# Performance work log

Measured on AMD Instinct MI355X. Metric: run time of the kernel, lower is better.

The kernel has to match this reference:

```python
import jax, jax.numpy as jnp
import numpy as np
from jax import lax

D = 300   # dim (hidden_size)
T = 1024  # grown history length
B = 128   # batched independent steps


def _conv(x, w, b):
    # NCHW conv, 3x3, stride 1, SAME padding (matches nn.Conv2d(.,.,3,1,1))
    return lax.conv_general_dilated(x, w, (1, 1), 'SAME',
                                    dimension_numbers=('NCHW', 'OIHW', 'NCHW')) + b[None, :, None, None]


def _bn(x, g, b, eps=1e-5):
    # eval-mode BatchNorm2d with running_mean=0, running_var=1
    return x * (g / jnp.sqrt(1.0 + eps))[None, :, None, None] + b[None, :, None, None]


def setup_inputs():
    key = jax.random.key(0)
    ks = iter(jax.random.split(key, 64))
    def rn(shape, scale=1.0):
        return jax.random.normal(next(ks), shape, dtype=jnp.float32) * scale
    inp = {
        'x': rn((B, D)),
        'hidden_states': rn((B, T, D)),
        'past_ht': rn((B, T, D)),
        'past_c': rn((B, T, D)),
        'W': rn((4 * D, 2 * D), 0.05),
        'b': rn((4 * D,)).at[:D].set(1.0),   # self.b[:dim] = 1
        'W_h': rn((10, D), 0.1),
        'W_x': rn((10, D), 0.1),
        'W_ht': rn((10, D), 0.1),
        'v': rn((10,)),
        'rb_w': rn((1600, 4 * D), 0.02),  # reshape_bef: Linear(1200, 1600)
        'rb_b': rn((1600,), 0.02),
        'rp_w': rn((4 * D, 1600), 0.02),  # reshape_pos: Linear(1600, 1200)
        'rp_b': rn((4 * D,), 0.02),
    }
    chans = [(1, 32), (32, 64), (64, 64), (64, 64), (64, 32), (32, 1)]
    for i, (ci, co) in enumerate(chans, 1):
        inp[f'c{i}_w'] = rn((co, ci, 3, 3), 0.1)
        inp[f'c{i}_b'] = rn((co,), 0.02)
        inp[f'c{i}_g'] = jnp.ones((co,), jnp.float32)
        inp[f'c{i}_beta'] = jnp.zeros((co,), jnp.float32)
    inp['pc_w'] = rn((1, 2, 3, 3), 0.1)
    inp['pc_b'] = rn((1,), 0.02)
    inp['pc_g'] = jnp.ones((1,), jnp.float32)
    inp['pc_beta'] = jnp.zeros((1,), jnp.float32)
    return inp


def reference(x, hidden_states, past_ht, past_c, W, b, W_h, W_x, W_ht, v,
              rb_w, rb_b, rp_w, rp_b,
              c1_w, c1_b, c1_g, c1_beta, c2_w, c2_b, c2_g, c2_beta,
              c3_w, c3_b, c3_g, c3_beta, c4_w, c4_b, c4_g, c4_beta,
              c5_w, c5_b, c5_g, c5_beta, c6_w, c6_b, c6_g, c6_beta,
              pc_w, pc_b, pc_g, pc_beta):
    # --- intra-attention over the grown history (vectorized over k) ---
    # a_k = v @ tanh(W_h h_k + W_x x + W_ht pht_k)
    e = jnp.tanh(jnp.einsum('btd,kd->btk', hidden_states, W_h)
                 + jnp.einsum('bd,kd->bk', x, W_x)[:, None, :]
                 + jnp.einsum('btd,kd->btk', past_ht, W_ht))
    s = jax.nn.softmax(jnp.einsum('btk,k->bt', e, v), axis=-1)
    ht = jnp.einsum('bt,btd->bd', s, hidden_states)
    ct = jnp.einsum('bt,btd->bd', s, past_c)
    # --- gate pre-activations ---
    whx = jnp.concatenate([ht, x], axis=-1) @ W.T + b          # [B, 1200]
    whx = whx @ rb_w.T + rb_b                                  # [B, 1600]
    pre = whx.reshape(-1, 1, 40, 40)
    # --- inter conv block (dropout is identity in eval) ---
    y = pre
    for (w, bi, g, be) in ((c1_w, c1_b, c1_g, c1_beta), (c2_w, c2_b, c2_g, c2_beta),
                           (c3_w, c3_b, c3_g, c3_beta), (c4_w, c4_b, c4_g, c4_beta),
                           (c5_w, c5_b, c5_g, c5_beta), (c6_w, c6_b, c6_g, c6_beta)):
        y = _bn(jax.nn.relu(_conv(y, w, bi)), g, be)
    y = _bn(_conv(jnp.concatenate([pre, y], axis=1), pc_w, pc_b), pc_g, pc_beta)
    whx = y.reshape(-1, 1600) @ rp_w.T + rp_b                  # [B, 1200]
    # --- LSTM gating ---
    f_t = jax.nn.sigmoid(whx[:, :D])
    o_t = jax.nn.sigmoid(whx[:, D:2 * D])
    i_t = jax.nn.sigmoid(whx[:, 2 * D:3 * D])
    ch_t = jnp.tanh(whx[:, 3 * D:4 * D])
    c = f_t * ct + i_t * ch_t
    h = o_t * jnp.tanh(c)
    return h
```

## Files before the change

kernel.cpp:

```cpp
#include <hip/hip_runtime.h>
#include <hip/hip_bf16.h>
#include <cstdint>
#include <cstddef>

typedef unsigned short u16;
typedef unsigned int u32;

#define DEV __device__ __forceinline__

DEV float bf2f(u16 u){ union{unsigned int i; float f;} c; c.i = ((unsigned)u)<<16; return c.f; }
DEV u16 f2bf(float f){ union{float f;unsigned int i;} c; c.f=f; unsigned int r = c.i + 0x7FFFu + ((c.i>>16)&1u); return (u16)(r>>16); }
DEV unsigned int pk2(float a, float b){
  __hip_bfloat162 t = __float22bfloat162_rn(float2{a,b});
  union { __hip_bfloat162 h; unsigned int u; } cv; cv.h = t; return cv.u;
}

typedef __attribute__((ext_vector_type(8))) short bf16x8;
typedef __attribute__((ext_vector_type(4))) float f32x4;
typedef __attribute__((ext_vector_type(8))) unsigned short us8v;

static constexpr size_t OFF_XW    = 0;
static constexpr size_t OFF_WHX2  = 8192;
static constexpr size_t OFF_WHX3  = OFF_WHX2 + (size_t)128*1600*4;
static constexpr size_t OFF_W21   = OFF_WHX3 + (size_t)128*1200*4;
static constexpr size_t OFF_WB2   = OFF_W21  + (size_t)288*4;
static constexpr size_t OFF_WB3   = OFF_WB2  + (size_t)18432*2;
static constexpr size_t OFF_WB4   = OFF_WB3  + (size_t)36864*2;
static constexpr size_t OFF_WB5   = OFF_WB4  + (size_t)36864*2;
static constexpr size_t OFF_W26   = OFF_WB5  + (size_t)18432*2;
static constexpr size_t OFF_PAR   = OFF_W26  + (size_t)288*4;
static constexpr size_t OFF_WPACK = OFF_PAR  + (size_t)6*768;
static constexpr size_t OFF_WB1G  = OFF_WPACK+ (size_t)20480*2;
static constexpr size_t OFF_RBWB  = OFF_WB1G + (size_t)1216*608*2;
static constexpr size_t OFF_RPWB  = OFF_RBWB + (size_t)1600*1216*2;
static constexpr size_t OFF_CAT   = OFF_RPWB + (size_t)1216*1600*2;
static constexpr size_t OFF_WHX1B = OFF_CAT  + (size_t)128*608*2;
static constexpr size_t OFF_O16B  = OFF_WHX1B+ (size_t)128*1216*2;
static constexpr size_t OFF_CT    = OFF_O16B + (size_t)128*1600*2;
static constexpr size_t OFF_A32   = OFF_CT   + (size_t)128*300*4;
static constexpr size_t OFF_B64   = OFF_A32  + (size_t)128*1764*32*2;
static constexpr size_t OFF_C64   = OFF_B64  + (size_t)128*1764*64*2;
static constexpr size_t OFF_P0    = OFF_C64  + (size_t)128*1764*64*2;
static constexpr size_t OFF_Y6    = OFF_P0   + (size_t)128*1764*2;
static constexpr size_t OFF_PART  = OFF_C64;

DEV void ring0(u16* buf, int j){
  int b = j/164, i = j%164;
  int y, x;
  if      (i < 42){ y = 0;        x = i; }
  else if (i < 84){ y = 41;       x = i-42; }
  else if (i < 124){ y = i-84+1;  x = 0; }
  else             { y = i-124+1; x = 41; }
  buf[(size_t)b*1764 + y*42 + x] = 0;
}
__global__ __launch_bounds__(256) void zero_mega(u16* __restrict__ p0, u16* __restrict__ y6,
                                                 u16* __restrict__ catb){
  int id = blockIdx.x*256 + threadIdx.x;
  if (id < 20992) ring0(p0, id);
  else if (id < 41984) ring0(y6, id-20992);
  else if (id < 42112){
    int b = id - 41984;
    us8v z = {0,0,0,0,0,0,0,0};
    *(us8v*)(catb + (size_t)b*608 + 600) = z;
  }
}

struct RArgs {
  const float* cw[6]; const float* cb[6]; const float* cg[6]; const float* cbe[6];
  const float* Wh; const float* Wht; const float* Wg; const float* rbw; const float* rpw;
  float* w21; float* w26; float* par;
  u16 *wb2, *wb3, *wb4, *wb5, *wpack, *Wb1, *rbwb, *rpwb;
};
DEV void cvW(const float* w, u16* dst, size_t j, int CI){
  int ci = j % CI; size_t rem = j / CI; int dydx = rem % 9; int co = rem / 9;
  dst[j] = f2bf(w[((size_t)co*CI + ci)*9 + dydx]);
}
__global__ __launch_bounds__(256) void mega_repack(RArgs a){
  const float isc = 1.0f/sqrtf(1.00001f);
  for (size_t id = (size_t)blockIdx.x*256 + threadIdx.x; id < 4762947ull;
       id += (size_t)gridDim.x*256){
    if (id < 288){
      int co = id % 32; size_t rem = id / 32; int k = rem % 9;
      a.w21[id] = a.cw[0][co*9 + k];
    } else if (id < 18720){ cvW(a.cw[1], a.wb2, id-288, 32); }
    else if (id < 55584){ cvW(a.cw[2], a.wb3, id-18720, 64); }
    else if (id < 92448){ cvW(a.cw[3], a.wb4, id-55584, 64); }
    else if (id < 110880){ cvW(a.cw[4], a.wb5, id-92448, 64); }
    else if (id < 111168){
      size_t j = id - 110880;
      a.w26[j] = a.cw[5][j];
    } else if (id < 131648){
      size_t j = id - 111168;
      int jj = j&7, col=(int)((j>>3)&15), kg=(int)((j>>7)&3); size_t rest=j>>9;
      int ks = (int)(rest%10), tz = (int)(rest/10);
      int k = ks*32 + kg*8 + jj;
      const float* src = tz ? a.Wht : a.Wh;
      a.wpack[j] = f2bf((col<10 && k<300)? src[col*300+k] : 0.f);
    } else if (id < 870976){
      size_t j = id - 131648; int k = (int)(j % 608); int n = (int)(j / 608);
      a.Wb1[j] = f2bf((n<1200 && k<600)? a.Wg[(size_t)n*600+k] : 0.f);
    } else if (id < 2816576){
      size_t j = id - 870976; int k = (int)(j % 1216); int n = (int)(j / 1216);
      a.rbwb[j] = f2bf((k<1200)? a.rbw[(size_t)n*1200+k] : 0.f);
    } else if (id < 4762176){
      size_t j = id - 2816576; int k = (int)(j % 1600); int n = (int)(j / 1600);
      a.rpwb[j] = f2bf((n<1200)? a.rpw[(size_t)n*1600+k] : 0.f);
    } else {
      size_t j = id - 4762176;
      int ci, CO; size_t base;
      if (j < 96){ ci=0; CO=32; base=0; }
      else if (j < 288){ ci=1; CO=64; base=96; }
      else if (j < 480){ ci=2; CO=64; base=288; }
      else if (j < 672){ ci=3; CO=64; base=480; }
      else if (j < 768){ ci=4; CO=32; base=672; }
      else { ci=5; CO=1; base=768; }
      size_t jj = j - base; int t = (int)(jj / CO); int c = (int)(jj % CO);
      float* p = a.par + (size_t)ci*192;
      p[t*CO + c] = (t==0)? a.cb[ci][c] : (t==1)? a.cg[ci][c]*isc : a.cbe[ci][c];
    }
  }
}

__global__ __launch_bounds__(64) void xw_k(const float* __restrict__ x, const float* __restrict__ Wx,
                                           float* __restrict__ xw){
  int id = blockIdx.x;
  int b = id/10, k = id%10;
  int lane = threadIdx.x;
  float a = 0.f;
  for (int d = lane; d < 300; d += 64)
    a = fmaf(x[b*300+d], Wx[k*300+d], a);
  #pragma unroll
  for (int off=1; off<64; off<<=1) a += __shfl_xor(a, off);
  if (lane==0) xw[b*16+k] = a;
}

__global__ __launch_bounds__(256,3) void attn_fused(const float* __restrict__ hs, const float* __restrict__ pht,
    const float* __restrict__ pc, const u16* __restrict__ wpack, const float* __restrict__ v,
    const float* __restrict__ xw, float* __restrict__ part){
  __shared__ u16 HL[32][328];
  __shared__ u16 PL[32][328];
  __shared__ float PS[2][32][18];
  __shared__ float PP[32];
  __shared__ float ML[2];
  int tid = threadIdx.x;
  int chunk = blockIdx.x, b = blockIdx.y;
  int rr0 = (b<<10) + chunk*32;
  const float* hsrc = hs  + (size_t)rr0*300;
  const float* psrc = pht + (size_t)rr0*300;
  const float* csrc = pc  + (size_t)rr0*300;
  float4 creg[10];
  #pragma unroll
  for (int rnd=0; rnd<10; rnd++){
    int idx = rnd*256 + tid;
    if (idx < 2400) creg[rnd] = *(const float4*)(csrc + idx*4);
  }
  #pragma unroll
  for (int rnd=0; rnd<10; rnd++){
    int idx = rnd*256 + tid;
    if (idx < 2400){
      float4 qh = *(const float4*)(hsrc + idx*4);
      float4 qp = *(const float4*)(psrc + idx*4);
      int row = idx/75, colp = (idx - row*75)*4;
      uint2 pvh; pvh.x = pk2(qh.x,qh.y); pvh.y = pk2(qh.z,qh.w);
      uint2 pvp; pvp.x = pk2(qp.x,qp.y); pvp.y = pk2(qp.z,qp.w);
      *(uint2*)(&HL[row][colp]) = pvh;
      *(uint2*)(&PL[row][colp]) = pvp;
    }
  }
  #pragma unroll
  for (int j=0;j<2;j++){
    int idx = j*256 + tid;
    if (idx < 448){
      int row = idx/14, cc = 300 + (idx - row*14)*2;
      *(u32*)(&HL[row][cc]) = 0u;
      *(u32*)(&PL[row][cc]) = 0u;
    }
  }
  __syncthreads();
  {
    int w = tid>>6, l = tid&63;
    int c = l&15, g = l>>4;
    int tz = w>>1, rf = w&1;
    const u16 (*SL)[328] = tz ? PL : HL;
    const u16* wbase = wpack + (size_t)tz*5120;
    f32x4 acc = (f32x4){0.f,0.f,0.f,0.f};
    #pragma unroll
    for (int ks=0; ks<10; ks++){
      bf16x8 af  = *(const bf16x8*)(&SL[rf*16 + c][ks*32 + g*8]);
      bf16x8 bfr = *(const bf16x8*)(wbase + ((ks*4 + g)*16 + c)*8);
      acc = __builtin_amdgcn_mfma_f32_16x16x32_bf16(af, bfr, acc, 0, 0, 0);
    }
    #pragma unroll
    for (int r=0;r<4;r++) PS[tz][rf*16 + g*4 + r][c] = acc[r];
  }
  __syncthreads();
  #pragma unroll
  for (int rnd=0; rnd<10; rnd++){
    int idx = rnd*256 + tid;
    if (idx < 2400){
      int row = idx/75, colp = (idx - row*75)*4;
      uint2 pv; pv.x = pk2(creg[rnd].x, creg[rnd].y); pv.y = pk2(creg[rnd].z, creg[rnd].w);
      *(uint2*)(&PL[row][colp]) = pv;
    }
  }
  if (tid < 32){
    float s = 0.f;
    #pragma unroll
    for (int k=0;k<10;k++)
      s += v[k]*tanhf(PS[0][tid][k] + PS[1][tid][k] + xw[b*16+k]);
    float m = s;
    #pragma unroll
    for (int off=1; off<32; off<<=1) m = fmaxf(m, __shfl_xor(m, off));
    float p = expf(s - m);
    float l = p;
    #pragma unroll
    for (int off=1; off<32; off<<=1) l += __shfl_xor(l, off);
    PP[tid] = p;
    if (tid==0){ ML[0]=m; ML[1]=l; }
  }
  __syncthreads();
  float* pp = part + ((size_t)b*32 + chunk)*608;
  if (tid < 150){
    int d = tid*2;
    float h0=0,h1=0,c0=0,c1=0;
    #pragma unroll
    for (int t=0;t<32;t++){
      float p = PP[t];
      u32 hw = *(const u32*)(&HL[t][d]);
      u32 cw = *(const u32*)(&PL[t][d]);
      h0 = fmaf(p, bf2f((u16)hw),       h0);
      h1 = fmaf(p, bf2f((u16)(hw>>16)), h1);
      c0 = fmaf(p, bf2f((u16)cw),       c0);
      c1 = fmaf(p, bf2f((u16)(cw>>16)), c1);
    }
    *(float2*)(pp + 4 + d)   = float2{h0,h1};
    *(float2*)(pp + 308 + d) = float2{c0,c1};
  }
  if (tid==0){ pp[0]=ML[0]; pp[1]=ML[1]; }
}

__global__ __launch_bounds__(192) void attn_reduce(const float* __restrict__ part,
    const float* __restrict__ x, float* __restrict__ ct, u16* __restrict__ catb){
  int b = blockIdx.x;
  int tid = threadIdx.x;
  const float* pb = part + (size_t)b*32*608;
  float M = -3.0e38f;
  #pragma unroll
  for (int j=0;j<32;j++) M = fmaxf(M, pb[j*608]);
  float L = 0.f;
  #pragma unroll
  for (int j=0;j<32;j++) L += pb[j*608+1]*expf(pb[j*608]-M);
  if (tid < 150){
    int d = tid*2;
    float a0=0,a1=0,b0=0,b1=0;
    #pragma unroll
    for (int j=0;j<32;j++){
      float w = expf(pb[j*608]-M);
      float2 hh = *(const float2*)(pb + j*608 + 4 + d);
      float2 cc = *(const float2*)(pb + j*608 + 308 + d);
      a0 = fmaf(w,hh.x,a0); a1 = fmaf(w,hh.y,a1);
      b0 = fmaf(w,cc.x,b0); b1 = fmaf(w,cc.y,b1);
    }
    float inv = 1.f/L;
    *(float2*)(ct + (size_t)b*300 + d) = float2{b0*inv, b1*inv};
    *(u32*)(catb + (size_t)b*608 + d)       = pk2(a0*inv, a1*inv);
    *(u32*)(catb + (size_t)b*608 + 300 + d) = pk2(x[(size_t)b*300 + d], x[(size_t)b*300 + d + 1]);
  }
}

template<int KP, bool OUTBF>
__global__ __launch_bounds__(256) void gemm_mfma(int NW, int NB, int ldo,
    const u16* __restrict__ inB, const u16* __restrict__ Wb,
    const float* __restrict__ bias, void* __restrict__ outp){
  __shared__ float red[4][64][4];
  int w = threadIdx.x>>6, l = threadIdx.x&63;
  int c = l&15, g = l>>4;
  int n0 = blockIdx.x*16;
  int b0 = blockIdx.y*16;
  const u16* arow = Wb  + (size_t)(n0 + c)*KP + g*8;
  const u16* brow = inB + (size_t)(b0 + c)*KP + g*8;
  f32x4 acc = (f32x4){0.f,0.f,0.f,0.f};
  for (int ks = w; ks < KP/32; ks += 4){
    bf16x8 af = *(const bf16x8*)(arow + ks*32);
    bf16x8 bf = *(const bf16x8*)(brow + ks*32);
    acc = __builtin_amdgcn_mfma_f32_16x16x32_bf16(af, bf, acc, 0, 0, 0);
  }
  #pragma unroll
  for (int r=0;r<4;r++) red[w][l][r] = acc[r];
  __syncthreads();
  if (w==0){
    float s0 = red[0][l][0]+red[1][l][0]+red[2][l][0]+red[3][l][0];
    float s1 = red[0][l][1]+red[1][l][1]+red[2][l][1]+red[3][l][1];
    float s2 = red[0][l][2]+red[1][l][2]+red[2][l][2]+red[3][l][2];
    float s3 = red[0][l][3]+red[1][l][3]+red[2][l][3]+red[3][l][3];
    int b = b0 + c, nb = n0 + g*4;
    if (nb < NW){
      float4 bi;
      if (nb < NB) bi = *(const float4*)(bias + nb);
      else { bi.x=0; bi.y=0; bi.z=0; bi.w=0; }
      float o0=s0+bi.x, o1=s1+bi.y, o2=s2+bi.z, o3=s3+bi.w;
      if (OUTBF){
        ushort4 st; st.x=f2bf(o0); st.y=f2bf(o1); st.z=f2bf(o2); st.w=f2bf(o3);
        *(ushort4*)((u16*)outp + (size_t)b*ldo + nb) = st;
      } else {
        float4 st; st.x=o0; st.y=o1; st.z=o2; st.w=o3;
        *(float4*)((float*)outp + (size_t)b*ldo + nb) = st;
      }
    }
  }
}

DEV void bzero(u16* buf, int j, int CH, int C){
  int c8 = j % CH; int rem = j / CH;
  int i = rem % 164, b = rem / 164;
  int y, x;
  if      (i < 42){ y = 0;        x = i; }
  else if (i < 84){ y = 41;       x = i-42; }
  else if (i < 124){ y = i-84+1;  x = 0; }
  else             { y = i-124+1; x = 41; }
  us8v z = {0,0,0,0,0,0,0,0};
  *(us8v*)(buf + ((size_t)b*1764 + y*42 + x)*C + c8*8) = z;
}
__global__ __launch_bounds__(256) void scat_border(const float* __restrict__ whx2, u16* __restrict__ p0,
    u16* __restrict__ A32, u16* __restrict__ B64, u16* __restrict__ C64){
  int id = blockIdx.x*256 + threadIdx.x;
  if (id < 204800){
    int b = id/1600, p = id%1600;
    int y = p/40, x = p%40;
    p0[(size_t)b*1764 + (y+1)*42 + (x+1)] = f2bf(whx2[id]);
  } else if (id < 288768){ bzero(A32, id-204800, 4, 32); }
  else if (id < 456704){ bzero(B64, id-288768, 8, 64); }
  else { bzero(C64, id-456704, 8, 64); }
}

template<int CI, int CO>
__global__ __launch_bounds__(256) void conv_tile(const u16* __restrict__ in, u16* __restrict__ out,
    const u16* __restrict__ wB, const float* __restrict__ par){
  constexpr int PCI  = CI + 8;
  constexpr int MF   = CO/16;
  constexpr int FPW  = MF;
  constexpr int KC   = CI/32;
  constexpr int KROW = CI*9;
  constexpr int CH8  = CI/8;
  __shared__ u16 TIN[100*PCI];
  int tile = blockIdx.x;
  int b = blockIdx.y;
  int y0 = (tile/5)*8, x0 = (tile%5)*8;
  const u16* inb = in + (size_t)b*1764*CI;
  for (int g = threadIdx.x; g < 100*CH8; g += 256){
    int pix = g/CH8, ch = g - pix*CH8;
    int r = pix/10, cc = pix - r*10;
    us8v vdat = *(const us8v*)(inb + ((size_t)(y0+r)*42 + (x0+cc))*CI + ch*8);
    *(us8v*)(&TIN[pix*PCI + ch*8]) = vdat;
  }
  __syncthreads();
  int w = threadIdx.x>>6, l = threadIdx.x&63;
  int c = l&15, kg = l>>4;
  int mg, f0;
  if (MF==4){ mg = w; f0 = 0; } else { mg = w&1; f0 = (w>>1)*2; }
  int pxb[FPW];
  #pragma unroll
  for (int fi=0; fi<FPW; fi++){
    int px = (f0+fi)*16 + c;
    int ty = px>>3, tx = px&7;
    pxb[fi] = (ty*10 + tx)*PCI + kg*8;
  }
  const u16* wrow = wB + (size_t)(mg*16 + c)*KROW;
  f32x4 acc[FPW];
  #pragma unroll
  for (int fi=0; fi<FPW; fi++) acc[fi] = (f32x4){0.f,0.f,0.f,0.f};
  #pragma unroll
  for (int dy=0;dy<3;dy++)
  #pragma unroll
  for (int dx=0;dx<3;dx++){
    int dydx = dy*3+dx;
    #pragma unroll
    for (int kc=0; kc<KC; kc++){
      bf16x8 af = *(const bf16x8*)(wrow + dydx*CI + kc*32 + kg*8);
      #pragma unroll
      for (int fi=0; fi<FPW; fi++){
        bf16x8 bf = *(const bf16x8*)(&TIN[pxb[fi] + (dy*10+dx)*PCI + kc*32]);
        acc[fi] = __builtin_amdgcn_mfma_f32_16x16x32_bf16(af, bf, acc[fi], 0, 0, 0);
      }
    }
  }
  u16* ob = out + (size_t)b*1764*CO;
  int co0 = mg*16 + kg*4;
  const float4 bia = *(const float4*)(par + co0);
  const float4 sc  = *(const float4*)(par + CO + co0);
  const float4 be  = *(const float4*)(par + 2*CO + co0);
  #pragma unroll
  for (int fi=0; fi<FPW; fi++){
    int px = (f0+fi)*16 + c;
    int y = y0 + (px>>3), x = x0 + (px&7);
    ushort4 s;
    s.x = f2bf(fmaxf(acc[fi][0]+bia.x,0.f)*sc.x + be.x);
    s.y = f2bf(fmaxf(acc[fi][1]+bia.y,0.f)*sc.y + be.y);
    s.z = f2bf(fmaxf(acc[fi][2]+bia.z,0.f)*sc.z + be.z);
    s.w = f2bf(fmaxf(acc[fi][3]+bia.w,0.f)*sc.w + be.w);
    *(ushort4*)(ob + (size_t)((y+1)*42 + (x+1))*CO + co0) = s;
  }
}

template<int CI, int CO, bool TT>
__global__ __launch_bounds__(256) void conv_main(const u16* __restrict__ in, u16* __restrict__ out,
    const float* __restrict__ w2, const float* __restrict__ par){
  int b = blockIdx.x;
  int wave = threadIdx.x >> 6;
  int lane = threadIdx.x & 63;
  int tile, co;
  if (TT){ tile = blockIdx.y*8 + wave*2 + (lane>>5); co = lane & 31; }
  else   { tile = blockIdx.y*4 + wave;               co = lane; }
  int y0 = (tile >> 3)*5, x0 = (tile & 7)*5;
  const u16* inb = in + (size_t)b*1764*CI;
  float acc[25];
  #pragma unroll
  for (int p=0;p<25;p++) acc[p]=0.f;
  for (int ci=0; ci<CI; ci++){
    float win[49];
    #pragma unroll
    for (int r=0;r<7;r++)
      #pragma unroll
      for (int c=0;c<7;c++)
        win[r*7+c] = bf2f(inb[ ((y0+r)*42 + (x0+c))*CI + ci ]);
    float wk[9];
    #pragma unroll
    for (int k=0;k<9;k++) wk[k] = w2[(ci*9+k)*CO + co];
    #pragma unroll
    for (int py=0;py<5;py++)
      #pragma unroll
      for (int px=0;px<5;px++){
        float s = acc[py*5+px];
        #pragma unroll
        for (int dy=0;dy<3;dy++)
          #pragma unroll
          for (int dx=0;dx<3;dx++)
            s = fmaf(wk[dy*3+dx], win[(py+dy)*7 + (px+dx)], s);
        acc[py*5+px] = s;
      }
  }
  float bia = par[co], sc = par[CO+co], be = par[2*CO+co];
  u16* outb = out + (size_t)b*1764*CO;
  #pragma unroll
  for (int py=0;py<5;py++)
    #pragma unroll
    for (int px=0;px<5;px++){
      float vv = fmaxf(acc[py*5+px] + bia, 0.f)*sc + be;
      outb[ ((y0+py+1)*42 + (x0+px+1))*CO + co ] = f2bf(vv);
    }
}

__global__ __launch_bounds__(256) void conv_c6(const u16* __restrict__ in, u16* __restrict__ y6,
    const float* __restrict__ w6, const float* __restrict__ par6){
  int id = blockIdx.x*256 + threadIdx.x;
  int b = id/1600, p = id%1600;
  int y = p/40, x = p%40;
  const u16* inb = in + (size_t)b*1764*32;
  float acc = 0.f;
  #pragma unroll
  for (int dy=0;dy<3;dy++)
    #pragma unroll
    for (int dx=0;dx<3;dx++){
      const u16* q = inb + ((y+dy)*42 + (x+dx))*32;
      int k = dy*3+dx;
      #pragma unroll
      for (int g=0; g<4; g++){
        us8v vv8 = *(const us8v*)(q + g*8);
        #pragma unroll
        for (int j=0;j<8;j++)
          acc = fmaf(w6[(g*8+j)*9 + k], bf2f(vv8[j]), acc);
      }
    }
  float vv = fmaxf(acc + par6[0], 0.f)*par6[1] + par6[2];
  y6[(size_t)b*1764 + (y+1)*42 + (x+1)] = f2bf(vv);
}

__global__ __launch_bounds__(256) void conv_pc(const u16* __restrict__ p0, const u16* __restrict__ y6,
    const float* __restrict__ pcw, const float* __restrict__ pcb,
    const float* __restrict__ pcg, const float* __restrict__ pcbe,
    u16* __restrict__ o16b){
  int id = blockIdx.x*256 + threadIdx.x;
  int b = id/1600, p = id%1600;
  int y = p/40, x = p%40;
  float acc = 0.f;
  #pragma unroll
  for (int dy=0;dy<3;dy++)
    #pragma unroll
    for (int dx=0;dx<3;dx++){
      size_t o = (size_t)b*1764 + (y+dy)*42 + (x+dx);
      acc = fmaf(pcw[dy*3+dx],     bf2f(p0[o]), acc);
      acc = fmaf(pcw[9 + dy*3+dx], bf2f(y6[o]), acc);
    }
  float sc = pcg[0] * (1.0f/sqrtf(1.00001f));
  o16b[id] = f2bf((acc + pcb[0])*sc + pcbe[0]);
}

__global__ __launch_bounds__(256) void gate_k(const float* __restrict__ whx3, const float* __restrict__ ct,
                                              float* __restrict__ outp){
  int id = blockIdx.x*256 + threadIdx.x;
  if (id >= 38400) return;
  int b = id/300, d = id%300;
  const float* r = whx3 + (size_t)b*1200;
  float ft = 1.f/(1.f+expf(-r[d]));
  float ot = 1.f/(1.f+expf(-r[300+d]));
  float it = 1.f/(1.f+expf(-r[600+d]));
  float ch = tanhf(r[900+d]);
  float c  = ft*ct[id] + it*ch;
  outp[id] = ot*tanhf(c);
}

extern "C" void kernel_launch(void* const* d_in, const int* in_sizes, int n_in,
                              void* d_out, int out_size, void* d_ws, size_t ws_size,
                              hipStream_t stream){
  const float* x    = (const float*)d_in[0];
  const float* hs   = (const float*)d_in[1];
  const float* pht  = (const float*)d_in[2];
  const float* pc   = (const float*)d_in[3];
  const float* W    = (const float*)d_in[4];
  const float* bb   = (const float*)d_in[5];
  const float* Wh   = (const float*)d_in[6];
  const float* Wx   = (const float*)d_in[7];
  const float* Wht  = (const float*)d_in[8];
  const float* v    = (const float*)d_in[9];
  const float* rbw  = (const float*)d_in[10];
  const float* rbb  = (const float*)d_in[11];
  const float* rpw  = (const float*)d_in[12];
  const float* rpb  = (const float*)d_in[13];
  const float *cw[6], *cb[6], *cg[6], *cbe[6];
  for (int i=0;i<6;i++){
    cw[i]=(const float*)d_in[14+4*i]; cb[i]=(const float*)d_in[15+4*i];
    cg[i]=(const float*)d_in[16+4*i]; cbe[i]=(const float*)d_in[17+4*i];
  }
  const float* pcw = (const float*)d_in[38];
  const float* pcb = (const float*)d_in[39];
  const float* pcg = (const float*)d_in[40];
  const float* pcbe= (const float*)d_in[41];

  char* ws = (char*)d_ws;
  float* xw    = (float*)(ws + OFF_XW);
  float* whx2  = (float*)(ws + OFF_WHX2);
  float* whx3  = (float*)(ws + OFF_WHX3);
  float* w21   = (float*)(ws + OFF_W21);
  u16*   wb2   = (u16*)  (ws + OFF_WB2);
  u16*   wb3   = (u16*)  (ws + OFF_WB3);
  u16*   wb4   = (u16*)  (ws + OFF_WB4);
  u16*   wb5   = (u16*)  (ws + OFF_WB5);
  float* w26   = (float*)(ws + OFF_W26);
  u16*   wpack = (u16*)  (ws + OFF_WPACK);
  u16*   wb1g  = (u16*)  (ws + OFF_WB1G);
  u16*   rbwb  = (u16*)  (ws + OFF_RBWB);
  u16*   rpwb  = (u16*)  (ws + OFF_RPWB);
  u16*   catb  = (u16*)  (ws + OFF_CAT);
  u16*   whx1b = (u16*)  (ws + OFF_WHX1B);
  u16*   o16b  = (u16*)  (ws + OFF_O16B);
  float* part  = (float*)(ws + OFF_PART);
  float* parb  = (float*)(ws + OFF_PAR);
  float* ct = (float*)(ws + OFF_CT);
  u16* A32 = (u16*)(ws + OFF_A32);
  u16* B64 = (u16*)(ws + OFF_B64);
  u16* C64 = (u16*)(ws + OFF_C64);
  u16* P0  = (u16*)(ws + OFF_P0);
  u16* Y6  = (u16*)(ws + OFF_Y6);

  RArgs ra;
  for (int i=0;i<6;i++){ ra.cw[i]=cw[i]; ra.cb[i]=cb[i]; ra.cg[i]=cg[i]; ra.cbe[i]=cbe[i]; }
  ra.Wh=Wh; ra.Wht=Wht; ra.Wg=W; ra.rbw=rbw; ra.rpw=rpw;
  ra.w21=w21; ra.w26=w26; ra.par=parb;
  ra.wb2=wb2; ra.wb3=wb3; ra.wb4=wb4; ra.wb5=wb5; ra.wpack=wpack;
  ra.Wb1=wb1g; ra.rbwb=rbwb; ra.rpwb=rpwb;

  zero_mega<<<165,256,0,stream>>>(P0, Y6, catb);
  mega_repack<<<2048,256,0,stream>>>(ra);

  xw_k<<<1280,64,0,stream>>>(x, Wx, xw);
  attn_fused<<<dim3(32,128),256,0,stream>>>(hs, pht, pc, wpack, v, xw, part);
  attn_reduce<<<128,192,0,stream>>>(part, x, ct, catb);

  gemm_mfma< 608,true ><<<dim3(76,8), 256,0,stream>>>(1216, 1200, 1216, catb,  wb1g, bb,  whx1b);
  gemm_mfma<1216,false><<<dim3(100,8),256,0,stream>>>(1600, 1600, 1600, whx1b, rbwb, rbb, whx2);
  scat_border<<<2440,256,0,stream>>>(whx2, P0, A32, B64, C64);

  conv_main<1,32,true><<<dim3(128,8),256,0,stream>>>(P0, A32, w21, parb);
  conv_tile<32,64><<<dim3(25,128),256,0,stream>>>(A32, B64, wb2, parb + 192);
  conv_tile<64,64><<<dim3(25,128),256,0,stream>>>(B64, C64, wb3, parb + 384);
  conv_tile<64,64><<<dim3(25,128),256,0,stream>>>(C64, B64, wb4, parb + 576);
  conv_tile<64,32><<<dim3(25,128),256,0,stream>>>(B64, A32, wb5, parb + 768);
  conv_c6<<<800,256,0,stream>>>(A32, Y6, w26, parb + 960);
  conv_pc<<<800,256,0,stream>>>(P0, Y6, pcw, pcb, pcg, pcbe, o16b);

  gemm_mfma<1600,false><<<dim3(75,8),256,0,stream>>>(1200, 1200, 1200, o16b, rpwb, rpb, whx3);
  gate_k<<<150,256,0,stream>>>(whx3, ct, (float*)d_out);
}
```

Baseline: 358.2 us.

## Merge attention, zeroing and weight repack into one launch; fuse scatter into GEMM epilogue

Attention chunk blocks, border-zeroing blocks and weight-repack blocks now run as branches of a single large grid, so the independent work overlaps inside one launch instead of running as separate kernels. The second GEMM writes bf16 directly into the padded P0 conv input, which removes the fp32 whx2 round trip and the scat_border kernel. The partial buffer moves to its own region so it no longer aliases C64, which is now zeroed concurrently. In exchange there is a new prep kernel for wpack/xw, and the GEMM epilogue now does scalar strided bf16 stores.

```diff
diff --git a/kernel.cpp b/kernel.cpp
--- a/kernel.cpp
+++ b/kernel.cpp
@@ -42,7 +42,8 @@
 static constexpr size_t OFF_C64   = OFF_B64  + (size_t)128*1764*64*2;
 static constexpr size_t OFF_P0    = OFF_C64  + (size_t)128*1764*64*2;
 static constexpr size_t OFF_Y6    = OFF_P0   + (size_t)128*1764*2;
-static constexpr size_t OFF_PART  = OFF_C64;
+static constexpr size_t OFF_PARTX = OFF_Y6   + (size_t)128*1764*2;
+static constexpr size_t OFF_END   = OFF_PARTX+ (size_t)128*32*608*4;
 
 DEV void ring0(u16* buf, int j){
   int b = j/164, i = j%164;
@@ -53,190 +54,210 @@
   else             { y = i-124+1; x = 41; }
   buf[(size_t)b*1764 + y*42 + x] = 0;
 }
-__global__ __launch_bounds__(256) void zero_mega(u16* __restrict__ p0, u16* __restrict__ y6,
-                                                 u16* __restrict__ catb){
-  int id = blockIdx.x*256 + threadIdx.x;
-  if (id < 20992) ring0(p0, id);
-  else if (id < 41984) ring0(y6, id-20992);
-  else if (id < 42112){
-    int b = id - 41984;
-    us8v z = {0,0,0,0,0,0,0,0};
-    *(us8v*)(catb + (size_t)b*608 + 600) = z;
-  }
-}
-
-struct RArgs {
-  const float* cw[6]; const float* cb[6]; const float* cg[6]; const float* cbe[6];
-  const float* Wh; const float* Wht; const float* Wg; const float* rbw; const float* rpw;
-  float* w21; float* w26; float* par;
-  u16 *wb2, *wb3, *wb4, *wb5, *wpack, *Wb1, *rbwb, *rpwb;
-};
+DEV void bzero(u16* buf, int j, int CH, int C){
+  int c8 = j % CH; int rem = j / CH;
+  int i = rem % 164, b = rem / 164;
+  int y, x;
+  if      (i < 42){ y = 0;        x = i; }
+  else if (i < 84){ y = 41;       x = i-42; }
+  else if (i < 124){ y = i-84+1;  x = 0; }
+  else             { y = i-124+1; x = 41; }
+  us8v z = {0,0,0,0,0,0,0,0};
+  *(us8v*)(buf + ((size_t)b*1764 + y*42 + x)*C + c8*8) = z;
+}
 DEV void cvW(const float* w, u16* dst, size_t j, int CI){
   int ci = j % CI; size_t rem = j / CI; int dydx = rem % 9; int co = rem / 9;
   dst[j] = f2bf(w[((size_t)co*CI + ci)*9 + dydx]);
 }
-__global__ __launch_bounds__(256) void mega_repack(RArgs a){
-  const float isc = 1.0f/sqrtf(1.00001f);
-  for (size_t id = (size_t)blockIdx.x*256 + threadIdx.x; id < 4762947ull;
-       id += (size_t)gridDim.x*256){
-    if (id < 288){
-      int co = id % 32; size_t rem = id / 32; int k = rem % 9;
-      a.w21[id] = a.cw[0][co*9 + k];
-    } else if (id < 18720){ cvW(a.cw[1], a.wb2, id-288, 32); }
-    else if (id < 55584){ cvW(a.cw[2], a.wb3, id-18720, 64); }
-    else if (id < 92448){ cvW(a.cw[3], a.wb4, id-55584, 64); }
-    else if (id < 110880){ cvW(a.cw[4], a.wb5, id-92448, 64); }
-    else if (id < 111168){
-      size_t j = id - 110880;
-      a.w26[j] = a.cw[5][j];
-    } else if (id < 131648){
-      size_t j = id - 111168;
-      int jj = j&7, col=(int)((j>>3)&15), kg=(int)((j>>7)&3); size_t rest=j>>9;
-      int ks = (int)(rest%10), tz = (int)(rest/10);
-      int k = ks*32 + kg*8 + jj;
-      const float* src = tz ? a.Wht : a.Wh;
-      a.wpack[j] = f2bf((col<10 && k<300)? src[col*300+k] : 0.f);
-    } else if (id < 870976){
-      size_t j = id - 131648; int k = (int)(j % 608); int n = (int)(j / 608);
-      a.Wb1[j] = f2bf((n<1200 && k<600)? a.Wg[(size_t)n*600+k] : 0.f);
-    } else if (id < 2816576){
-      size_t j = id - 870976; int k = (int)(j % 1216); int n = (int)(j / 1216);
-      a.rbwb[j] = f2bf((k<1200)? a.rbw[(size_t)n*1200+k] : 0.f);
-    } else if (id < 4762176){
-      size_t j = id - 2816576; int k = (int)(j % 1600); int n = (int)(j / 1600);
-      a.rpwb[j] = f2bf((n<1200)? a.rpw[(size_t)n*1600+k] : 0.f);
-    } else {
-      size_t j = id - 4762176;
-      int ci, CO; size_t base;
-      if (j < 96){ ci=0; CO=32; base=0; }
-      else if (j < 288){ ci=1; CO=64; base=96; }
-      else if (j < 480){ ci=2; CO=64; base=288; }
-      else if (j < 672){ ci=3; CO=64; base=480; }
-      else if (j < 768){ ci=4; CO=32; base=672; }
-      else { ci=5; CO=1; base=768; }
-      size_t jj = j - base; int t = (int)(jj / CO); int c = (int)(jj % CO);
-      float* p = a.par + (size_t)ci*192;
-      p[t*CO + c] = (t==0)? a.cb[ci][c] : (t==1)? a.cg[ci][c]*isc : a.cbe[ci][c];
-    }
-  }
-}
-
-__global__ __launch_bounds__(64) void xw_k(const float* __restrict__ x, const float* __restrict__ Wx,
-                                           float* __restrict__ xw){
-  int id = blockIdx.x;
-  int b = id/10, k = id%10;
-  int lane = threadIdx.x;
-  float a = 0.f;
-  for (int d = lane; d < 300; d += 64)
-    a = fmaf(x[b*300+d], Wx[k*300+d], a);
-  #pragma unroll
-  for (int off=1; off<64; off<<=1) a += __shfl_xor(a, off);
-  if (lane==0) xw[b*16+k] = a;
-}
-
-__global__ __launch_bounds__(256,3) void attn_fused(const float* __restrict__ hs, const float* __restrict__ pht,
-    const float* __restrict__ pc, const u16* __restrict__ wpack, const float* __restrict__ v,
-    const float* __restrict__ xw, float* __restrict__ part){
-  __shared__ u16 HL[32][328];
-  __shared__ u16 PL[32][328];
-  __shared__ float PS[2][32][18];
-  __shared__ float PP[32];
-  __shared__ float ML[2];
+
+__global__ __launch_bounds__(256) void prep_k(const float* __restrict__ Wh, const float* __restrict__ Wht,
+    const float* __restrict__ x, const float* __restrict__ Wx,
+    u16* __restrict__ wp, float* __restrict__ xw){
+  int bid = blockIdx.x, tid = threadIdx.x;
+  if (bid < 80){
+    int j = bid*256 + tid;
+    int jj = j&7, col=(j>>3)&15, kg=(j>>7)&3, rest=j>>9;
+    int ks = rest%10, tz = rest/10;
+    int k = ks*32 + kg*8 + jj;
+    const float* src = tz ? Wht : Wh;
+    wp[j] = f2bf((col<10 && k<300)? src[col*300+k] : 0.f);
+  } else {
+    int gw = (bid-80)*4 + (tid>>6);
+    int lane = tid & 63;
+    int b = gw/10, k = gw%10;
+    float a = 0.f;
+    for (int d = lane; d < 300; d += 64)
+      a = fmaf(x[b*300+d], Wx[k*300+d], a);
+    #pragma unroll
+    for (int off=1; off<64; off<<=1) a += __shfl_xor(a, off);
+    if (lane==0) xw[b*16+k] = a;
+  }
+}
+
+struct MArgs {
+  const float *hs, *pht, *pc, *v, *xw;
+  const u16* wpack;
+  float* part;
+  const float* cw0; const float* cw1; const float* cw2; const float* cw3; const float* cw4; const float* cw5;
+  const float* cb[6]; const float* cg[6]; const float* cbe[6];
+  const float* Wg; const float* rbw; const float* rpw;
+  float* w21; float* w26; float* par;
+  u16 *wb2, *wb3, *wb4, *wb5, *Wb1, *rbwb, *rpwb;
+  u16 *p0, *y6, *catb, *A32, *B64, *C64;
+};
+__global__ __launch_bounds__(256,3) void attn_mega(MArgs a){
+  int bid = blockIdx.x;
   int tid = threadIdx.x;
-  int chunk = blockIdx.x, b = blockIdx.y;
-  int rr0 = (b<<10) + chunk*32;
-  const float* hsrc = hs  + (size_t)rr0*300;
-  const float* psrc = pht + (size_t)rr0*300;
-  const float* csrc = pc  + (size_t)rr0*300;
-  float4 creg[10];
-  #pragma unroll
-  for (int rnd=0; rnd<10; rnd++){
-    int idx = rnd*256 + tid;
-    if (idx < 2400) creg[rnd] = *(const float4*)(csrc + idx*4);
-  }
-  #pragma unroll
-  for (int rnd=0; rnd<10; rnd++){
-    int idx = rnd*256 + tid;
-    if (idx < 2400){
-      float4 qh = *(const float4*)(hsrc + idx*4);
-      float4 qp = *(const float4*)(psrc + idx*4);
-      int row = idx/75, colp = (idx - row*75)*4;
-      uint2 pvh; pvh.x = pk2(qh.x,qh.y); pvh.y = pk2(qh.z,qh.w);
-      uint2 pvp; pvp.x = pk2(qp.x,qp.y); pvp.y = pk2(qp.z,qp.w);
-      *(uint2*)(&HL[row][colp]) = pvh;
-      *(uint2*)(&PL[row][colp]) = pvp;
-    }
-  }
-  #pragma unroll
-  for (int j=0;j<2;j++){
-    int idx = j*256 + tid;
-    if (idx < 448){
-      int row = idx/14, cc = 300 + (idx - row*14)*2;
-      *(u32*)(&HL[row][cc]) = 0u;
-      *(u32*)(&PL[row][cc]) = 0u;
-    }
-  }
-  __syncthreads();
-  {
-    int w = tid>>6, l = tid&63;
-    int c = l&15, g = l>>4;
-    int tz = w>>1, rf = w&1;
-    const u16 (*SL)[328] = tz ? PL : HL;
-    const u16* wbase = wpack + (size_t)tz*5120;
-    f32x4 acc = (f32x4){0.f,0.f,0.f,0.f};
-    #pragma unroll
-    for (int ks=0; ks<10; ks++){
-      bf16x8 af  = *(const bf16x8*)(&SL[rf*16 + c][ks*32 + g*8]);
-      bf16x8 bfr = *(const bf16x8*)(wbase + ((ks*4 + g)*16 + c)*8);
-      acc = __builtin_amdgcn_mfma_f32_16x16x32_bf16(af, bfr, acc, 0, 0, 0);
-    }
-    #pragma unroll
-    for (int r=0;r<4;r++) PS[tz][rf*16 + g*4 + r][c] = acc[r];
-  }
-  __syncthreads();
-  #pragma unroll
-  for (int rnd=0; rnd<10; rnd++){
-    int idx = rnd*256 + tid;
-    if (idx < 2400){
-      int row = idx/75, colp = (idx - row*75)*4;
-      uint2 pv; pv.x = pk2(creg[rnd].x, creg[rnd].y); pv.y = pk2(creg[rnd].z, creg[rnd].w);
-      *(uint2*)(&PL[row][colp]) = pv;
-    }
-  }
-  if (tid < 32){
-    float s = 0.f;
-    #pragma unroll
-    for (int k=0;k<10;k++)
-      s += v[k]*tanhf(PS[0][tid][k] + PS[1][tid][k] + xw[b*16+k]);
-    float m = s;
-    #pragma unroll
-    for (int off=1; off<32; off<<=1) m = fmaxf(m, __shfl_xor(m, off));
-    float p = expf(s - m);
-    float l = p;
-    #pragma unroll
-    for (int off=1; off<32; off<<=1) l += __shfl_xor(l, off);
-    PP[tid] = p;
-    if (tid==0){ ML[0]=m; ML[1]=l; }
-  }
-  __syncthreads();
-  float* pp = part + ((size_t)b*32 + chunk)*608;
-  if (tid < 150){
-    int d = tid*2;
-    float h0=0,h1=0,c0=0,c1=0;
-    #pragma unroll
-    for (int t=0;t<32;t++){
-      float p = PP[t];
-      u32 hw = *(const u32*)(&HL[t][d]);
-      u32 cw = *(const u32*)(&PL[t][d]);
-      h0 = fmaf(p, bf2f((u16)hw),       h0);
-      h1 = fmaf(p, bf2f((u16)(hw>>16)), h1);
-      c0 = fmaf(p, bf2f((u16)cw),       c0);
-      c1 = fmaf(p, bf2f((u16)(cw>>16)), c1);
-    }
-    *(float2*)(pp + 4 + d)   = float2{h0,h1};
-    *(float2*)(pp + 308 + d) = float2{c0,c1};
-  }
-  if (tid==0){ pp[0]=ML[0]; pp[1]=ML[1]; }
+  if (bid < 4096){
+    __shared__ u16 HL[32][328];
+    __shared__ u16 PL[32][328];
+    __shared__ float PS[2][32][18];
+    __shared__ float PP[32];
+    __shared__ float ML[2];
+    int chunk = bid & 31, b = bid >> 5;
+    int rr0 = (b<<10) + chunk*32;
+    const float* hsrc = a.hs  + (size_t)rr0*300;
+    const float* psrc = a.pht + (size_t)rr0*300;
+    const float* csrc = a.pc  + (size_t)rr0*300;
+    float4 creg[10];
+    #pragma unroll
+    for (int rnd=0; rnd<10; rnd++){
+      int idx = rnd*256 + tid;
+      if (idx < 2400) creg[rnd] = *(const float4*)(csrc + idx*4);
+    }
+    #pragma unroll
+    for (int rnd=0; rnd<10; rnd++){
+      int idx = rnd*256 + tid;
+      if (idx < 2400){
+        float4 qh = *(const float4*)(hsrc + idx*4);
+        float4 qp = *(const float4*)(psrc + idx*4);
+        int row = idx/75, colp = (idx - row*75)*4;
+        uint2 pvh; pvh.x = pk2(qh.x,qh.y); pvh.y = pk2(qh.z,qh.w);
+        uint2 pvp; pvp.x = pk2(qp.x,qp.y); pvp.y = pk2(qp.z,qp.w);
+        *(uint2*)(&HL[row][colp]) = pvh;
+        *(uint2*)(&PL[row][colp]) = pvp;
+      }
+    }
+    #pragma unroll
+    for (int j=0;j<2;j++){
+      int idx = j*256 + tid;
+      if (idx < 448){
+        int row = idx/14, cc = 300 + (idx - row*14)*2;
+        *(u32*)(&HL[row][cc]) = 0u;
+        *(u32*)(&PL[row][cc]) = 0u;
+      }
+    }
+    __syncthreads();
+    {
+      int w = tid>>6, l = tid&63;
+      int c = l&15, g = l>>4;
+      int tz = w>>1, rf = w&1;
+      const u16 (*SL)[328] = tz ? PL : HL;
+      const u16* wbase = a.wpack + (size_t)tz*5120;
+      f32x4 acc = (f32x4){0.f,0.f,0.f,0.f};
+      #pragma unroll
+      for (int ks=0; ks<10; ks++){
+        bf16x8 af  = *(const bf16x8*)(&SL[rf*16 + c][ks*32 + g*8]);
+        bf16x8 bfr = *(const bf16x8*)(wbase + ((ks*4 + g)*16 + c)*8);
+        acc = __builtin_amdgcn_mfma_f32_16x16x32_bf16(af, bfr, acc, 0, 0, 0);
+      }
+      #pragma unroll
+      for (int r=0;r<4;r++) PS[tz][rf*16 + g*4 + r][c] = acc[r];
+    }
+    __syncthreads();
+    #pragma unroll
+    for (int rnd=0; rnd<10; rnd++){
+      int idx = rnd*256 + tid;
+      if (idx < 2400){
+        int row = idx/75, colp = (idx - row*75)*4;
+        uint2 pv; pv.x = pk2(creg[rnd].x, creg[rnd].y); pv.y = pk2(creg[rnd].z, creg[rnd].w);
+        *(uint2*)(&PL[row][colp]) = pv;
+      }
+    }
+    if (tid < 32){
+      float s = 0.f;
+      #pragma unroll
+      for (int k=0;k<10;k++)
+        s += a.v[k]*tanhf(PS[0][tid][k] + PS[1][tid][k] + a.xw[b*16+k]);
+      float m = s;
+      #pragma unroll
+      for (int off=1; off<32; off<<=1) m = fmaxf(m, __shfl_xor(m, off));
+      float p = expf(s - m);
+      float l = p;
+      #pragma unroll
+      for (int off=1; off<32; off<<=1) l += __shfl_xor(l, off);
+      PP[tid] = p;
+      if (tid==0){ ML[0]=m; ML[1]=l; }
+    }
+    __syncthreads();
+    float* pp = a.part + ((size_t)b*32 + chunk)*608;
+    if (tid < 150){
+      int d = tid*2;
+      float h0=0,h1=0,c0=0,c1=0;
+      #pragma unroll
+      for (int t=0;t<32;t++){
+        float p = PP[t];
+        u32 hw = *(const u32*)(&HL[t][d]);
+        u32 cw = *(const u32*)(&PL[t][d]);
+        h0 = fmaf(p, bf2f((u16)hw),       h0);
+        h1 = fmaf(p, bf2f((u16)(hw>>16)), h1);
+        c0 = fmaf(p, bf2f((u16)cw),       c0);
+        c1 = fmaf(p, bf2f((u16)(cw>>16)), c1);
+      }
+      *(float2*)(pp + 4 + d)   = float2{h0,h1};
+      *(float2*)(pp + 308 + d) = float2{c0,c1};
+    }
+    if (tid==0){ pp[0]=ML[0]; pp[1]=ML[1]; }
+  } else if (bid < 5901){
+    int zid = (bid-4096)*256 + tid;
+    if (zid < 20992) ring0(a.p0, zid);
+    else if (zid < 41984) ring0(a.y6, zid-20992);
+    else if (zid < 42112){
+      int b = zid - 41984;
+      us8v z = {0,0,0,0,0,0,0,0};
+      *(us8v*)(a.catb + (size_t)b*608 + 600) = z;
+    }
+    else if (zid < 126080){ bzero(a.A32, zid-42112, 4, 32); }
+    else if (zid < 294016){ bzero(a.B64, zid-126080, 8, 64); }
+    else if (zid < 461952){ bzero(a.C64, zid-294016, 8, 64); }
+  } else {
+    const float isc = 1.0f/sqrtf(1.00001f);
+    const float* cwA[6] = {a.cw0,a.cw1,a.cw2,a.cw3,a.cw4,a.cw5};
+    for (size_t id = (size_t)(bid-5901)*256 + tid; id < 4742467ull; id += (size_t)512*256){
+      if (id < 288){
+        int co = id % 32; size_t rem = id / 32; int k = rem % 9;
+        a.w21[id] = cwA[0][co*9 + k];
+      } else if (id < 18720){ cvW(cwA[1], a.wb2, id-288, 32); }
+      else if (id < 55584){ cvW(cwA[2], a.wb3, id-18720, 64); }
+      else if (id < 92448){ cvW(cwA[3], a.wb4, id-55584, 64); }
+      else if (id < 110880){ cvW(cwA[4], a.wb5, id-92448, 64); }
+      else if (id < 111168){
+        size_t j = id - 110880;
+        a.w26[j] = cwA[5][j];
+      } else if (id < 850496){
+        size_t j = id - 111168; int k = (int)(j % 608); int n = (int)(j / 608);
+        a.Wb1[j] = f2bf((n<1200 && k<600)? a.Wg[(size_t)n*600+k] : 0.f);
+      } else if (id < 2796096){
+        size_t j = id - 850496; int k = (int)(j % 1216); int n = (int)(j / 1216);
+        a.rbwb[j] = f2bf((k<1200)? a.rbw[(size_t)n*1200+k] : 0.f);
+      } else if (id < 4741696){
+        size_t j = id - 2796096; int k = (int)(j % 1600); int n = (int)(j / 1600);
+        a.rpwb[j] = f2bf((n<1200)? a.rpw[(size_t)n*1600+k] : 0.f);
+      } else {
+        size_t j = id - 4741696;
+        int ci, CO; size_t base;
+        if (j < 96){ ci=0; CO=32; base=0; }
+        else if (j < 288){ ci=1; CO=64; base=96; }
+        else if (j < 480){ ci=2; CO=64; base=288; }
+        else if (j < 672){ ci=3; CO=64; base=480; }
+        else if (j < 768){ ci=4; CO=32; base=672; }
+        else { ci=5; CO=1; base=768; }
+        size_t jj = j - base; int t = (int)(jj / CO); int c = (int)(jj % CO);
+        float* p = a.par + (size_t)ci*192;
+        p[t*CO + c] = (t==0)? a.cb[ci][c] : (t==1)? a.cg[ci][c]*isc : a.cbe[ci][c];
+      }
+    }
+  }
 }
 
 __global__ __launch_bounds__(192) void attn_reduce(const float* __restrict__ part,
@@ -268,7 +289,7 @@
   }
 }
 
-template<int KP, bool OUTBF>
+template<int KP, int OMODE>
 __global__ __launch_bounds__(256) void gemm_mfma(int NW, int NB, int ldo,
     const u16* __restrict__ inB, const u16* __restrict__ Wb,
     const float* __restrict__ bias, void* __restrict__ outp){
@@ -299,7 +320,11 @@
       if (nb < NB) bi = *(const float4*)(bias + nb);
       else { bi.x=0; bi.y=0; bi.z=0; bi.w=0; }
       float o0=s0+bi.x, o1=s1+bi.y, o2=s2+bi.z, o3=s3+bi.w;
-      if (OUTBF){
+      if (OMODE==2){
+        int row = nb/40, col = nb%40;
+        u16* pp0 = (u16*)outp + (size_t)b*1764 + (row+1)*42 + (col+1);
+        pp0[0]=f2bf(o0); pp0[1]=f2bf(o1); pp0[2]=f2bf(o2); pp0[3]=f2bf(o3);
+      } else if (OMODE==1){
         ushort4 st; st.x=f2bf(o0); st.y=f2bf(o1); st.z=f2bf(o2); st.w=f2bf(o3);
         *(ushort4*)((u16*)outp + (size_t)b*ldo + nb) = st;
       } else {
@@ -308,29 +333,6 @@
       }
     }
   }
-}
-
-DEV void bzero(u16* buf, int j, int CH, int C){
-  int c8 = j % CH; int rem = j / CH;
-  int i = rem % 164, b = rem / 164;
-  int y, x;
-  if      (i < 42){ y = 0;        x = i; }
-  else if (i < 84){ y = 41;       x = i-42; }
-  else if (i < 124){ y = i-84+1;  x = 0; }
-  else             { y = i-124+1; x = 41; }
-  us8v z = {0,0,0,0,0,0,0,0};
-  *(us8v*)(buf + ((size_t)b*1764 + y*42 + x)*C + c8*8) = z;
-}
-__global__ __launch_bounds__(256) void scat_border(const float* __restrict__ whx2, u16* __restrict__ p0,
-    u16* __restrict__ A32, u16* __restrict__ B64, u16* __restrict__ C64){
-  int id = blockIdx.x*256 + threadIdx.x;
-  if (id < 204800){
-    int b = id/1600, p = id%1600;
-    int y = p/40, x = p%40;
-    p0[(size_t)b*1764 + (y+1)*42 + (x+1)] = f2bf(whx2[id]);
-  } else if (id < 288768){ bzero(A32, id-204800, 4, 32); }
-  else if (id < 456704){ bzero(B64, id-288768, 8, 64); }
-  else { bzero(C64, id-456704, 8, 64); }
 }
 
 template<int CI, int CO>
@@ -538,7 +540,6 @@
 
   char* ws = (char*)d_ws;
   float* xw    = (float*)(ws + OFF_XW);
-  float* whx2  = (float*)(ws + OFF_WHX2);
   float* whx3  = (float*)(ws + OFF_WHX3);
   float* w21   = (float*)(ws + OFF_W21);
   u16*   wb2   = (u16*)  (ws + OFF_WB2);
@@ -553,7 +554,7 @@
   u16*   catb  = (u16*)  (ws + OFF_CAT);
   u16*   whx1b = (u16*)  (ws + OFF_WHX1B);
   u16*   o16b  = (u16*)  (ws + OFF_O16B);
-  float* part  = (float*)(ws + OFF_PART);
+  float* part  = (float*)(ws + OFF_PARTX);
   float* parb  = (float*)(ws + OFF_PAR);
   float* ct = (float*)(ws + OFF_CT);
   u16* A32 = (u16*)(ws + OFF_A32);
@@ -562,23 +563,22 @@
   u16* P0  = (u16*)(ws + OFF_P0);
   u16* Y6  = (u16*)(ws + OFF_Y6);
 
-  RArgs ra;
-  for (int i=0;i<6;i++){ ra.cw[i]=cw[i]; ra.cb[i]=cb[i]; ra.cg[i]=cg[i]; ra.cbe[i]=cbe[i]; }
-  ra.Wh=Wh; ra.Wht=Wht; ra.Wg=W; ra.rbw=rbw; ra.rpw=rpw;
-  ra.w21=w21; ra.w26=w26; ra.par=parb;
-  ra.wb2=wb2; ra.wb3=wb3; ra.wb4=wb4; ra.wb5=wb5; ra.wpack=wpack;
-  ra.Wb1=wb1g; ra.rbwb=rbwb; ra.rpwb=rpwb;
-
-  zero_mega<<<165,256,0,stream>>>(P0, Y6, catb);
-  mega_repack<<<2048,256,0,stream>>>(ra);
-
-  xw_k<<<1280,64,0,stream>>>(x, Wx, xw);
-  attn_fused<<<dim3(32,128),256,0,stream>>>(hs, pht, pc, wpack, v, xw, part);
+  MArgs ma;
+  ma.hs=hs; ma.pht=pht; ma.pc=pc; ma.v=v; ma.xw=xw; ma.wpack=wpack; ma.part=part;
+  ma.cw0=cw[0]; ma.cw1=cw[1]; ma.cw2=cw[2]; ma.cw3=cw[3]; ma.cw4=cw[4]; ma.cw5=cw[5];
+  for (int i=0;i<6;i++){ ma.cb[i]=cb[i]; ma.cg[i]=cg[i]; ma.cbe[i]=cbe[i]; }
+  ma.Wg=W; ma.rbw=rbw; ma.rpw=rpw;
+  ma.w21=w21; ma.w26=w26; ma.par=parb;
+  ma.wb2=wb2; ma.wb3=wb3; ma.wb4=wb4; ma.wb5=wb5;
+  ma.Wb1=wb1g; ma.rbwb=rbwb; ma.rpwb=rpwb;
+  ma.p0=P0; ma.y6=Y6; ma.catb=catb; ma.A32=A32; ma.B64=B64; ma.C64=C64;
+
+  prep_k<<<400,256,0,stream>>>(Wh, Wht, x, Wx, wpack, xw);
+  attn_mega<<<6413,256,0,stream>>>(ma);
   attn_reduce<<<128,192,0,stream>>>(part, x, ct, catb);
 
-  gemm_mfma< 608,true ><<<dim3(76,8), 256,0,stream>>>(1216, 1200, 1216, catb,  wb1g, bb,  whx1b);
-  gemm_mfma<1216,false><<<dim3(100,8),256,0,stream>>>(1600, 1600, 1600, whx1b, rbwb, rbb, whx2);
-  scat_border<<<2440,256,0,stream>>>(whx2, P0, A32, B64, C64);
+  gemm_mfma< 608,1><<<dim3(76,8), 256,0,stream>>>(1216, 1200, 1216, catb,  wb1g, bb,  whx1b);
+  gemm_mfma<1216,2><<<dim3(100,8),256,0,stream>>>(1600, 1600, 0,    whx1b, rbwb, rbb, P0);
 
   conv_main<1,32,true><<<dim3(128,8),256,0,stream>>>(P0, A32, w21, parb);
   conv_tile<32,64><<<dim3(25,128),256,0,stream>>>(A32, B64, wb2, parb + 192);
@@ -588,6 +588,6 @@
   conv_c6<<<800,256,0,stream>>>(A32, Y6, w26, parb + 960);
   conv_pc<<<800,256,0,stream>>>(P0, Y6, pcw, pcb, pcg, pcbe, o16b);
 
-  gemm_mfma<1600,false><<<dim3(75,8),256,0,stream>>>(1200, 1200, 1200, o16b, rpwb, rpb, whx3);
+  gemm_mfma<1600,0><<<dim3(75,8),256,0,stream>>>(1200, 1200, 1200, o16b, rpwb, rpb, whx3);
   gate_k<<<150,256,0,stream>>>(whx3, ct, (float*)d_out);
 }
```

After: 352.9 us, median of 2. Within noise of the previous version (-1.5%).
